# Optimization experiments

Hardware: AMD Instinct MI355X
Metric: run time of the kernel (lower is better)

## Reference

```python
import jax, jax.numpy as jnp
import numpy as np

B, S, K, D, H, COND, MR = 4, 1024, 1024, 1024, 16, 1024, 4
HD = D // H  # 64
INV_SQRT_HD = 1.0 / float(np.sqrt(HD))
GELU_C = 0.7978845608028654  # sqrt(2/pi)


def _make_rope(seqlen):
    pos = jnp.arange(seqlen, dtype=jnp.float32)
    inv = 1.0 / (10000.0 ** (jnp.arange(0, HD // 2, dtype=jnp.float32) * 2.0 / HD))
    ang = pos[:, None] * inv[None, :]                     # [S, HD/2]
    cos = jnp.concatenate([jnp.cos(ang), jnp.cos(ang)], -1)  # [S, HD]
    sin = jnp.concatenate([jnp.sin(ang), jnp.sin(ang)], -1)
    return cos[None, :, None, :], sin[None, :, None, :]   # [1,S,1,HD]


def setup_inputs():
    key = jax.random.key(0)
    ks = jax.random.split(key, 14)
    rn = lambda k, shape, s=0.02: jax.random.normal(k, shape, jnp.float32) * s
    cos_q, sin_q = _make_rope(S)
    cos_k, sin_k = _make_rope(K)
    ada_b = jnp.zeros((6 * D,), jnp.float32)
    ada_b = ada_b.at[2 * D:3 * D].set(0.5).at[5 * D:6 * D].set(0.5)  # gate_msa, gate_mlp init
    return {
        "q_x": jax.random.normal(ks[0], (B, S, D), jnp.float32),
        "kv_x": jax.random.normal(ks[1], (B, K, D), jnp.float32),
        "t_cond": jax.random.normal(ks[2], (B, COND), jnp.float32),
        "cos_q": cos_q, "sin_q": sin_q, "cos_k": cos_k, "sin_k": sin_k,
        "group_idxs": jax.random.randint(ks[3], (B, S), 0, 4, jnp.int32),
        "query_enabled": jax.random.randint(ks[4], (B, S), 0, 2, jnp.int32).astype(bool),
        "qn_w": jnp.ones((D,), jnp.float32),
        "kvn_w": jnp.ones((D,), jnp.float32),
        "n2_w": jnp.ones((D,), jnp.float32),
        "Wq": rn(ks[5], (D, D)), "Wkv": rn(ks[6], (D, 2 * D)), "Wo": rn(ks[7], (D, D)),
        "W1": rn(ks[8], (D, MR * D)), "b1": jnp.zeros((MR * D,), jnp.float32),
        "W2": rn(ks[9], (MR * D, D)), "b2": jnp.zeros((D,), jnp.float32),
        "adaW": rn(ks[10], (COND, 6 * D)), "adab": ada_b,
    }


def layer_norm(x, w):
    mu = jnp.mean(x, -1, keepdims=True)
    var = jnp.var(x, -1, keepdims=True)
    return (x - mu) * jax.lax.rsqrt(var + 1e-5) * w


def rope(x, cos, sin):
    # x: [B,S,H,HD]; cos/sin: [1,S,1,HD]; rotate_half convention
    x1, x2 = jnp.split(x, 2, axis=-1)
    return x * cos + jnp.concatenate([-x2, x1], -1) * sin


def gelu_tanh(x):
    return 0.5 * x * (1.0 + jnp.tanh(GELU_C * (x + 0.044715 * x * x * x)))


def reference(q_x, kv_x, t_cond, cos_q, sin_q, cos_k, sin_k, group_idxs, query_enabled,
              qn_w, kvn_w, n2_w, Wq, Wkv, Wo, W1, b1, W2, b2, adaW, adab):
    # adaLN modulation (inference: dropout disabled -> bias_dropout_add_scale = scale*x + residual)
    mod = (t_cond @ adaW + adab)[:, None, :]               # [B,1,6D]
    sh_msa, sc_msa, g_msa, sh_mlp, sc_mlp, g_mlp = jnp.split(mod, 6, axis=-1)

    qn = layer_norm(q_x, qn_w)
    kvn = layer_norm(kv_x, kvn_w)
    qn = qn * (1.0 + sc_msa) + sh_msa                      # modulate_fused

    q = (qn @ Wq).reshape(B, S, H, HD)
    kv = (kvn @ Wkv).reshape(B, K, 2, H, HD)
    k, v = kv[:, :, 0], kv[:, :, 1]
    q = rope(q, cos_q, sin_q)
    k = rope(k, cos_k, sin_k)

    # group cross-attn mask: attend only where groups differ
    attend = group_idxs[:, :, None] != group_idxs[:, None, :]  # [B,S,K]
    scores = jnp.einsum('bqhd,bkhd->bhqk', q, k) * INV_SQRT_HD
    scores = jnp.where(attend[:, None, :, :], scores, -1e9)
    p = jax.nn.softmax(scores, axis=-1)
    attn = jnp.einsum('bhqk,bkhd->bqhd', p, v).reshape(B, S, D)

    x = g_msa * (attn @ Wo) + q_x                          # fused bias-dropout-add-scale (inference)
    gate = query_enabled[..., None].astype(x.dtype)
    x = x * gate + q_x * (1.0 - gate)                      # gated_update

    x_mid = x
    h = layer_norm(x, n2_w) * (1.0 + sc_mlp) + sh_mlp
    h = gelu_tanh(h @ W1 + b1) @ W2 + b2
    x = g_mlp * h + x_mid
    x = x * gate + x_mid * (1.0 - gate)
    return x
```

## Files before the change

### kernel.cpp

```cpp
#include <hip/hip_runtime.h>
#include <hip/hip_bf16.h>
#include <math.h>

typedef __bf16 bf16_t;
typedef __attribute__((ext_vector_type(8))) __bf16 bf16x8;
typedef __attribute__((ext_vector_type(4))) float f32x4;

__global__ __launch_bounds__(256) void mod_init_kernel(
    const float* __restrict__ adab, float* __restrict__ mod)
{
  int i = blockIdx.x * 256 + threadIdx.x;
  int b = i / 6144, c = i - b * 6144;
  mod[i] = adab[c];
  (void)b;
}

__global__ __launch_bounds__(256) void mod_partial_kernel(
    const float* __restrict__ tc, const float* __restrict__ adaW,
    float* __restrict__ mod)
{
  __shared__ float st[4][128];
  int tid = threadIdx.x, z = blockIdx.y;
  for (int i = tid; i < 512; i += 256)
    st[i >> 7][i & 127] = tc[(i >> 7) * 1024 + z * 128 + (i & 127)];
  __syncthreads();
  int col = blockIdx.x * 256 + tid;
  float a0 = 0.f, a1 = 0.f, a2 = 0.f, a3 = 0.f;
  for (int k = 0; k < 128; ++k) {
    float wv = adaW[(size_t)(z * 128 + k) * 6144 + col];
    a0 = fmaf(st[0][k], wv, a0);
    a1 = fmaf(st[1][k], wv, a1);
    a2 = fmaf(st[2][k], wv, a2);
    a3 = fmaf(st[3][k], wv, a3);
  }
  atomicAdd(&mod[col], a0);
  atomicAdd(&mod[6144 + col], a1);
  atomicAdd(&mod[2 * 6144 + col], a2);
  atomicAdd(&mod[3 * 6144 + col], a3);
}

__global__ __launch_bounds__(256) void transpose_to_bf16(
    const float* __restrict__ in, bf16_t* __restrict__ out, int R, int C)
{
  __shared__ float tile[32][33];
  int c0 = blockIdx.x * 32, r0 = blockIdx.y * 32;
  int tx = threadIdx.x, ty = threadIdx.y;
#pragma unroll
  for (int i = 0; i < 4; ++i)
    tile[ty + i * 8][tx] = in[(size_t)(r0 + ty + i * 8) * C + c0 + tx];
  __syncthreads();
#pragma unroll
  for (int i = 0; i < 4; ++i)
    out[(size_t)(c0 + ty + i * 8) * R + r0 + tx] = (bf16_t)tile[tx][ty + i * 8];
}

__global__ __launch_bounds__(256) void ln_mod_kernel(
    const float* __restrict__ x, const float* __restrict__ wgt,
    const float* __restrict__ mod, int useMod, int shOff, int scOff,
    bf16_t* __restrict__ out)
{
  int row = blockIdx.x;
  int b = row >> 10;
  int tid = threadIdx.x;
  const float* xr = x + (size_t)row * 1024;
  float4 v = ((const float4*)xr)[tid];
  float s = v.x + v.y + v.z + v.w;
  float s2 = v.x * v.x + v.y * v.y + v.z * v.z + v.w * v.w;
#pragma unroll
  for (int off = 32; off > 0; off >>= 1) {
    s += __shfl_down(s, off, 64);
    s2 += __shfl_down(s2, off, 64);
  }
  __shared__ float ps[4], ps2[4];
  if ((tid & 63) == 0) { ps[tid >> 6] = s; ps2[tid >> 6] = s2; }
  __syncthreads();
  float mu = (ps[0] + ps[1] + ps[2] + ps[3]) * (1.0f / 1024.0f);
  float var = (ps2[0] + ps2[1] + ps2[2] + ps2[3]) * (1.0f / 1024.0f) - mu * mu;
  float rs = rsqrtf(var + 1e-5f);
  float xv[4] = {v.x, v.y, v.z, v.w};
#pragma unroll
  for (int i = 0; i < 4; ++i) {
    int col = tid * 4 + i;
    float n = (xv[i] - mu) * rs * wgt[col];
    if (useMod)
      n = n * (1.0f + mod[b * 6144 + scOff + col]) + mod[b * 6144 + shOff + col];
    out[(size_t)row * 1024 + col] = (bf16_t)n;
  }
}

__global__ __launch_bounds__(256) void reduce_q_rope_kernel(
    const float* __restrict__ P0, const float* __restrict__ P1,
    const float* __restrict__ cosq, const float* __restrict__ sinq,
    bf16_t* __restrict__ qr)
{
  int t = blockIdx.x * 256 + threadIdx.x;
  int hd = t & 31;
  int h = (t >> 5) & 15;
  int s = (t >> 9) & 1023;
  int b = t >> 19;
  size_t base = ((size_t)(b * 1024 + s)) * 1024 + h * 64 + hd;
  float v1 = P0[base] + P1[base];
  float v2 = P0[base + 32] + P1[base + 32];
  float c1 = cosq[s * 64 + hd], s1 = sinq[s * 64 + hd];
  float c2 = cosq[s * 64 + hd + 32], s2 = sinq[s * 64 + hd + 32];
  float o1 = (v1 * c1 - v2 * s1) * 0.125f;
  float o2 = (v2 * c2 + v1 * s2) * 0.125f;
  size_t ob = ((size_t)(b * 16 + h) * 1024 + s) * 64 + hd;
  qr[ob] = (bf16_t)o1;
  qr[ob + 32] = (bf16_t)o2;
}

__global__ __launch_bounds__(256) void reduce_kv_kernel(
    const float* __restrict__ P0, const float* __restrict__ P1,
    const float* __restrict__ cosk, const float* __restrict__ sink,
    bf16_t* __restrict__ kr, bf16_t* __restrict__ vt)
{
  __shared__ float ks[64][65];
  __shared__ float vs[64][65];
  int bh = blockIdx.x;
  int b = bh >> 4, h = bh & 15;
  int n0 = blockIdx.y * 64;
  int tid = threadIdx.x;
#pragma unroll
  for (int it = 0; it < 16; ++it) {
    int linear = tid + it * 256;
    int nl = linear >> 6, hd = linear & 63;
    size_t gi = ((size_t)(b * 1024 + n0 + nl)) * 2048 + h * 64 + hd;
    ks[nl][hd] = P0[gi] + P1[gi];
    vs[hd][nl] = P0[gi + 1024] + P1[gi + 1024];
  }
  __syncthreads();
#pragma unroll
  for (int it = 0; it < 16; ++it) {
    int linear = tid + it * 256;
    int nl = linear >> 6, hd = linear & 63;
    float kv = ks[nl][hd];
    float pv = ks[nl][hd ^ 32];
    float c = cosk[(n0 + nl) * 64 + hd], sn = sink[(n0 + nl) * 64 + hd];
    float o = (hd < 32) ? (kv * c - pv * sn) : (kv * c + pv * sn);
    kr[((size_t)bh * 1024 + n0 + nl) * 64 + hd] = (bf16_t)o;
    int rh = linear >> 6, nn = linear & 63;
    vt[((size_t)bh * 64 + rh) * 1024 + n0 + nn] = (bf16_t)vs[rh][nn];
  }
}

__global__ __launch_bounds__(256, 2) void attn_kernel(
    const bf16_t* __restrict__ qr, const bf16_t* __restrict__ kr,
    const bf16_t* __restrict__ vt, const int* __restrict__ grp,
    bf16_t* __restrict__ outp)
{
  __shared__ bf16_t Ks[64 * 72];
  __shared__ bf16_t Vs[64 * 72];
  __shared__ bf16_t Ps[128 * 72];
  __shared__ int gk[64];
  const int bh = blockIdx.x;
  const int b = bh >> 4, h = bh & 15;
  const int qBase = blockIdx.y * 128;
  const int tid = threadIdx.x, lane = tid & 63, w = tid >> 6;
  const int l15 = lane & 15, l4 = lane >> 4;
  const f32x4 zero = {0.f, 0.f, 0.f, 0.f};

  bf16x8 qA0[2], qA1[2];
  int gqr[2][4];
#pragma unroll
  for (int s = 0; s < 2; ++s) {
    int row = qBase + w * 32 + s * 16;
    const bf16_t* qp = qr + ((size_t)bh * 1024 + row + l15) * 64;
    qA0[s] = *(const bf16x8*)(qp + l4 * 8);
    qA1[s] = *(const bf16x8*)(qp + 32 + l4 * 8);
#pragma unroll
    for (int r = 0; r < 4; ++r) gqr[s][r] = grp[b * 1024 + row + l4 * 4 + r];
  }

  f32x4 oacc[2][4];
  float rsum[2][4];
#pragma unroll
  for (int s = 0; s < 2; ++s)
#pragma unroll
    for (int i = 0; i < 4; ++i) { oacc[s][i] = zero; rsum[s][i] = 0.f; }

  for (int kt = 0; kt < 16; ++kt) {
    __syncthreads();
#pragma unroll
    for (int i = 0; i < 2; ++i) {
      int c = tid * 2 + i;
      int r = c >> 3, cc = (c & 7) * 8;
      *(bf16x8*)(Ks + r * 72 + cc) =
          *(const bf16x8*)(kr + ((size_t)bh * 1024 + kt * 64 + r) * 64 + cc);
      *(bf16x8*)(Vs + r * 72 + cc) =
          *(const bf16x8*)(vt + ((size_t)bh * 64 + r) * 1024 + kt * 64 + cc);
    }
    if (tid < 64) gk[tid] = grp[b * 1024 + kt * 64 + tid];
    __syncthreads();

    int gkv[4];
    bf16x8 kf0[4], kf1[4];
#pragma unroll
    for (int nt = 0; nt < 4; ++nt) {
      gkv[nt] = gk[nt * 16 + l15];
      kf0[nt] = *(const bf16x8*)(Ks + (nt * 16 + l15) * 72 + l4 * 8);
      kf1[nt] = *(const bf16x8*)(Ks + (nt * 16 + l15) * 72 + 32 + l4 * 8);
    }

#pragma unroll
    for (int s = 0; s < 2; ++s) {
      f32x4 sacc[4];
#pragma unroll
      for (int nt = 0; nt < 4; ++nt) sacc[nt] = zero;
#pragma unroll
      for (int nt = 0; nt < 4; ++nt) {
        sacc[nt] = __builtin_amdgcn_mfma_f32_16x16x32_bf16(qA0[s], kf0[nt], sacc[nt], 0, 0, 0);
        sacc[nt] = __builtin_amdgcn_mfma_f32_16x16x32_bf16(qA1[s], kf1[nt], sacc[nt], 0, 0, 0);
      }
#pragma unroll
      for (int r = 0; r < 4; ++r) {
        int gq = gqr[s][r];
        float acc = 0.f;
#pragma unroll
        for (int nt = 0; nt < 4; ++nt) {
          float sv = sacc[nt][r] + ((gq == gkv[nt]) ? -60.f : 0.f);
          float p = __expf(sv);
          acc += p;
          Ps[(w * 32 + s * 16 + l4 * 4 + r) * 72 + nt * 16 + l15] = (bf16_t)p;
        }
        rsum[s][r] += acc;
      }
    }
    __syncthreads();
#pragma unroll
    for (int s = 0; s < 2; ++s) {
      const bf16_t* pp = Ps + (w * 32 + s * 16 + l15) * 72;
      bf16x8 pf0 = *(const bf16x8*)(pp + l4 * 8);
      bf16x8 pf1 = *(const bf16x8*)(pp + 32 + l4 * 8);
#pragma unroll
      for (int nt = 0; nt < 4; ++nt) {
        bf16x8 vf0 = *(const bf16x8*)(Vs + (nt * 16 + l15) * 72 + l4 * 8);
        bf16x8 vf1 = *(const bf16x8*)(Vs + (nt * 16 + l15) * 72 + 32 + l4 * 8);
        oacc[s][nt] = __builtin_amdgcn_mfma_f32_16x16x32_bf16(pf0, vf0, oacc[s][nt], 0, 0, 0);
        oacc[s][nt] = __builtin_amdgcn_mfma_f32_16x16x32_bf16(pf1, vf1, oacc[s][nt], 0, 0, 0);
      }
    }
  }

#pragma unroll
  for (int s = 0; s < 2; ++s)
#pragma unroll
    for (int r = 0; r < 4; ++r) {
      float t = rsum[s][r];
      t += __shfl_xor(t, 1, 64);
      t += __shfl_xor(t, 2, 64);
      t += __shfl_xor(t, 4, 64);
      t += __shfl_xor(t, 8, 64);
      rsum[s][r] = 1.f / t;
    }
#pragma unroll
  for (int s = 0; s < 2; ++s)
#pragma unroll
    for (int r = 0; r < 4; ++r) {
      int srow = qBase + w * 32 + s * 16 + l4 * 4 + r;
      float inv = rsum[s][r];
#pragma unroll
      for (int nt = 0; nt < 4; ++nt)
        outp[((size_t)(b * 1024 + srow)) * 1024 + h * 64 + nt * 16 + l15] =
            (bf16_t)(oacc[s][nt][r] * inv);
    }
}

__device__ __forceinline__ void stage16(const bf16_t* gp, bf16_t* lp) {
  __builtin_amdgcn_global_load_lds(
      (__attribute__((address_space(1))) void*)gp,
      (__attribute__((address_space(3))) void*)lp, 16, 0, 0);
}

template <int EPI>
__global__ __launch_bounds__(256, 2) void gemm_bt(
    const bf16_t* __restrict__ A, const bf16_t* __restrict__ Bt,
    int M, int N, int Kd, int kChunk,
    float* __restrict__ Cf, bf16_t* __restrict__ Cb,
    const float* __restrict__ bias)
{
  __shared__ bf16_t sA[128 * 32];
  __shared__ bf16_t sB[128 * 32];
  const int tid = threadIdx.x;
  const int lane = tid & 63, w = tid >> 6;
  const int wr = w >> 1, wc = w & 1;
  const int rowBase = blockIdx.y * 128;
  const int colBase = blockIdx.x * 128;
  const int l15 = lane & 15, l4 = lane >> 4;
  const int sr = lane >> 2;
  const int scc = (((lane & 3) ^ ((sr >> 1) & 3))) * 8;
  const int l4s = l4 ^ ((l15 >> 1) & 3);

  const f32x4 zero = {0.f, 0.f, 0.f, 0.f};
  f32x4 acc[4][4];
#pragma unroll
  for (int i = 0; i < 4; ++i)
#pragma unroll
    for (int j = 0; j < 4; ++j) acc[i][j] = zero;

  const bf16_t* aBase = A + (size_t)(rowBase + w * 32 + sr) * Kd + scc;
  const bf16_t* bBase = Bt + (size_t)(colBase + w * 32 + sr) * Kd + scc;

  const int kStart = blockIdx.z * kChunk;
  for (int k0 = kStart; k0 < kStart + kChunk; k0 += 32) {
    __syncthreads();
#pragma unroll
    for (int i = 0; i < 2; ++i) {
      stage16(aBase + (size_t)i * 16 * Kd + k0, sA + (w * 32 + i * 16) * 32);
      stage16(bBase + (size_t)i * 16 * Kd + k0, sB + (w * 32 + i * 16) * 32);
    }
    __syncthreads();
    bf16x8 af[4], bfr[4];
#pragma unroll
    for (int mt = 0; mt < 4; ++mt)
      af[mt] = *(const bf16x8*)(sA + (wr * 64 + mt * 16 + l15) * 32 + l4s * 8);
#pragma unroll
    for (int nt = 0; nt < 4; ++nt)
      bfr[nt] = *(const bf16x8*)(sB + (wc * 64 + nt * 16 + l15) * 32 + l4s * 8);
#pragma unroll
    for (int mt = 0; mt < 4; ++mt)
#pragma unroll
      for (int nt = 0; nt < 4; ++nt)
        acc[mt][nt] = __builtin_amdgcn_mfma_f32_16x16x32_bf16(af[mt], bfr[nt],
                                                              acc[mt][nt], 0, 0, 0);
  }

  const size_t zOff = (size_t)blockIdx.z * M * N;
#pragma unroll
  for (int mt = 0; mt < 4; ++mt) {
#pragma unroll
    for (int nt = 0; nt < 4; ++nt) {
      int col = colBase + wc * 64 + nt * 16 + l15;
#pragma unroll
      for (int r = 0; r < 4; ++r) {
        int rr = rowBase + wr * 64 + mt * 16 + l4 * 4 + r;
        float v = acc[mt][nt][r];
        if constexpr (EPI == 1) {
          float t = v + bias[col];
          float g = 0.5f * t *
                    (1.0f + tanhf(0.7978845608028654f * (t + 0.044715f * t * t * t)));
          Cb[(size_t)rr * N + col] = (bf16_t)g;
        } else {
          Cf[zOff + (size_t)rr * N + col] = v;
        }
      }
    }
  }
}

__global__ __launch_bounds__(256) void ln2_fused_kernel(
    const float* __restrict__ P0, const float* __restrict__ P1,
    const float* __restrict__ qx, const float* __restrict__ n2w,
    const float* __restrict__ mod, const int* __restrict__ qen,
    float* __restrict__ xbuf, bf16_t* __restrict__ xnmod)
{
  int row = blockIdx.x;
  int b = row >> 10;
  int tid = threadIdx.x;
  bool en = qen[row] != 0;
  float4 p0 = ((const float4*)(P0 + (size_t)row * 1024))[tid];
  float4 p1 = ((const float4*)(P1 + (size_t)row * 1024))[tid];
  float4 res = ((const float4*)(qx + (size_t)row * 1024))[tid];
  float4 g = ((const float4*)(mod + b * 6144 + 2048))[tid];
  float4 x;
  x.x = en ? fmaf(g.x, p0.x + p1.x, res.x) : res.x;
  x.y = en ? fmaf(g.y, p0.y + p1.y, res.y) : res.y;
  x.z = en ? fmaf(g.z, p0.z + p1.z, res.z) : res.z;
  x.w = en ? fmaf(g.w, p0.w + p1.w, res.w) : res.w;
  ((float4*)(xbuf + (size_t)row * 1024))[tid] = x;

  float s = x.x + x.y + x.z + x.w;
  float s2 = x.x * x.x + x.y * x.y + x.z * x.z + x.w * x.w;
#pragma unroll
  for (int off = 32; off > 0; off >>= 1) {
    s += __shfl_down(s, off, 64);
    s2 += __shfl_down(s2, off, 64);
  }
  __shared__ float ps[4], ps2[4];
  if ((tid & 63) == 0) { ps[tid >> 6] = s; ps2[tid >> 6] = s2; }
  __syncthreads();
  float mu = (ps[0] + ps[1] + ps[2] + ps[3]) * (1.0f / 1024.0f);
  float var = (ps2[0] + ps2[1] + ps2[2] + ps2[3]) * (1.0f / 1024.0f) - mu * mu;
  float rs = rsqrtf(var + 1e-5f);
  float4 sc = ((const float4*)(mod + b * 6144 + 4096))[tid];
  float4 sh = ((const float4*)(mod + b * 6144 + 3072))[tid];
  float4 wv = ((const float4*)n2w)[tid];
  float xv[4] = {x.x, x.y, x.z, x.w};
  float scv[4] = {sc.x, sc.y, sc.z, sc.w};
  float shv[4] = {sh.x, sh.y, sh.z, sh.w};
  float wvv[4] = {wv.x, wv.y, wv.z, wv.w};
#pragma unroll
  for (int i = 0; i < 4; ++i) {
    float n = (xv[i] - mu) * rs * wvv[i];
    n = n * (1.0f + scv[i]) + shv[i];
    xnmod[(size_t)row * 1024 + tid * 4 + i] = (bf16_t)n;
  }
}

__global__ __launch_bounds__(256) void final_reduce_kernel(
    const float* __restrict__ P, const float* __restrict__ b2,
    const float* __restrict__ mod, const int* __restrict__ qen,
    const float* __restrict__ xbuf, float* __restrict__ out)
{
  int row = blockIdx.x;
  int b = row >> 10;
  int tid = threadIdx.x;
  bool en = qen[row] != 0;
  size_t ro = (size_t)row * 1024;
  float4 p0 = ((const float4*)(P + ro))[tid];
  float4 p1 = ((const float4*)(P + 4194304 + ro))[tid];
  float4 p2 = ((const float4*)(P + 2 * 4194304 + ro))[tid];
  float4 p3 = ((const float4*)(P + 3 * 4194304 + ro))[tid];
  float4 bb = ((const float4*)b2)[tid];
  float4 xm = ((const float4*)(xbuf + ro))[tid];
  float4 g = ((const float4*)(mod + b * 6144 + 5120))[tid];
  float4 o;
  o.x = en ? fmaf(g.x, p0.x + p1.x + p2.x + p3.x + bb.x, xm.x) : xm.x;
  o.y = en ? fmaf(g.y, p0.y + p1.y + p2.y + p3.y + bb.y, xm.y) : xm.y;
  o.z = en ? fmaf(g.z, p0.z + p1.z + p2.z + p3.z + bb.z, xm.z) : xm.z;
  o.w = en ? fmaf(g.w, p0.w + p1.w + p2.w + p3.w + bb.w, xm.w) : xm.w;
  ((float4*)(out + ro))[tid] = o;
}

extern "C" void kernel_launch(void* const* d_in, const int* in_sizes, int n_in,
                              void* d_out, int out_size, void* d_ws, size_t ws_size,
                              hipStream_t stream)
{
  const float* q_x    = (const float*)d_in[0];
  const float* kv_x   = (const float*)d_in[1];
  const float* t_cond = (const float*)d_in[2];
  const float* cos_q  = (const float*)d_in[3];
  const float* sin_q  = (const float*)d_in[4];
  const float* cos_k  = (const float*)d_in[5];
  const float* sin_k  = (const float*)d_in[6];
  const int*   grp    = (const int*)d_in[7];
  const int*   qen    = (const int*)d_in[8];
  const float* qn_w   = (const float*)d_in[9];
  const float* kvn_w  = (const float*)d_in[10];
  const float* n2_w   = (const float*)d_in[11];
  const float* Wq     = (const float*)d_in[12];
  const float* Wkv    = (const float*)d_in[13];
  const float* Wo     = (const float*)d_in[14];
  const float* W1     = (const float*)d_in[15];
  const float* b1     = (const float*)d_in[16];
  const float* W2     = (const float*)d_in[17];
  const float* b2     = (const float*)d_in[18];
  const float* adaW   = (const float*)d_in[19];
  const float* adab   = (const float*)d_in[20];
  float* out = (float*)d_out;

  char* ws = (char*)d_ws;
  const size_t MB = 1ull << 20;
  float*  mod    = (float*)(ws + 0);
  bf16_t* Wq_t   = (bf16_t*)(ws + 98304);
  bf16_t* Wkv_t  = (bf16_t*)(ws + 98304 + 2 * MB);
  bf16_t* Wo_t   = (bf16_t*)(ws + 98304 + 6 * MB);
  bf16_t* W1_t   = (bf16_t*)(ws + 98304 + 8 * MB);
  bf16_t* W2_t   = (bf16_t*)(ws + 98304 + 16 * MB);
  bf16_t* qn_mod = (bf16_t*)(ws + 98304 + 24 * MB);
  bf16_t* kvn    = (bf16_t*)(ws + 98304 + 32 * MB);
  bf16_t* q_r    = (bf16_t*)(ws + 98304 + 40 * MB);
  bf16_t* k_r    = (bf16_t*)(ws + 98304 + 48 * MB);
  bf16_t* v_t    = (bf16_t*)(ws + 98304 + 56 * MB);
  bf16_t* h1     = (bf16_t*)(ws + 98304 + 64 * MB);
  float*  scr    = (float*)(ws + 98304 + 96 * MB);
  bf16_t* xn_mod = qn_mod;
  bf16_t* attn_o = kvn;
  float*  xbuf   = (float*)q_r;

  mod_init_kernel<<<96, 256, 0, stream>>>(adab, mod);
  mod_partial_kernel<<<dim3(24, 8), 256, 0, stream>>>(t_cond, adaW, mod);
  transpose_to_bf16<<<dim3(32, 32),  dim3(32, 8), 0, stream>>>(Wq,  Wq_t,  1024, 1024);
  transpose_to_bf16<<<dim3(64, 32),  dim3(32, 8), 0, stream>>>(Wkv, Wkv_t, 1024, 2048);
  transpose_to_bf16<<<dim3(32, 32),  dim3(32, 8), 0, stream>>>(Wo,  Wo_t,  1024, 1024);
  transpose_to_bf16<<<dim3(128, 32), dim3(32, 8), 0, stream>>>(W1,  W1_t,  1024, 4096);
  transpose_to_bf16<<<dim3(32, 128), dim3(32, 8), 0, stream>>>(W2,  W2_t,  4096, 1024);
  ln_mod_kernel<<<4096, 256, 0, stream>>>(q_x,  qn_w,  mod, 1, 0, 1024, qn_mod);
  ln_mod_kernel<<<4096, 256, 0, stream>>>(kv_x, kvn_w, mod, 0, 0, 0,    kvn);
  gemm_bt<4><<<dim3(8, 32, 2), 256, 0, stream>>>(qn_mod, Wq_t, 4096, 1024, 1024, 512,
                                                 scr, nullptr, nullptr);
  reduce_q_rope_kernel<<<8192, 256, 0, stream>>>(scr, scr + 4194304, cos_q, sin_q, q_r);
  gemm_bt<4><<<dim3(16, 32, 2), 256, 0, stream>>>(kvn, Wkv_t, 4096, 2048, 1024, 512,
                                                  scr, nullptr, nullptr);
  reduce_kv_kernel<<<dim3(64, 16), 256, 0, stream>>>(scr, scr + 8388608, cos_k, sin_k,
                                                     k_r, v_t);
  attn_kernel<<<dim3(64, 8), 256, 0, stream>>>(q_r, k_r, v_t, grp, attn_o);
  gemm_bt<4><<<dim3(8, 32, 2), 256, 0, stream>>>(attn_o, Wo_t, 4096, 1024, 1024, 512,
                                                 scr, nullptr, nullptr);
  ln2_fused_kernel<<<4096, 256, 0, stream>>>(scr, scr + 4194304, q_x, n2_w, mod, qen,
                                             xbuf, xn_mod);
  gemm_bt<1><<<dim3(32, 32, 1), 256, 0, stream>>>(xn_mod, W1_t, 4096, 4096, 1024, 1024,
                                                  nullptr, h1, b1);
  gemm_bt<4><<<dim3(8, 32, 4), 256, 0, stream>>>(h1, W2_t, 4096, 1024, 4096, 1024,
                                                 scr, nullptr, nullptr);
  final_reduce_kernel<<<4096, 256, 0, stream>>>(scr, b2, mod, qen, xbuf, out);
}
```

Before: 484.0 us.

## Store split-K partials in bf16, remap GEMM tiles per XCD, use exp-based GELU

Split-K GEMM partial outputs are now written and read as bf16 instead of fp32, halving scratch traffic for all reduce/epilogue kernels. The GEMM block index is remapped so blocks landing on the same XCD cover a contiguous region of tiles, aiming for better L2 reuse. The GELU tanh is replaced by an __expf-based formula. Storing partials in bf16 before summation loses precision, and the tile remapping assumes grid dimensions divisible by 8, 4 and 2.

```diff
diff --git a/kernel.cpp b/kernel.cpp
--- a/kernel.cpp
+++ b/kernel.cpp
@@ -4,6 +4,7 @@
 
 typedef __bf16 bf16_t;
 typedef __attribute__((ext_vector_type(8))) __bf16 bf16x8;
+typedef __attribute__((ext_vector_type(4))) __bf16 bf16x4;
 typedef __attribute__((ext_vector_type(4))) float f32x4;
 
 __global__ __launch_bounds__(256) void mod_init_kernel(
@@ -89,7 +90,7 @@
 }
 
 __global__ __launch_bounds__(256) void reduce_q_rope_kernel(
-    const float* __restrict__ P0, const float* __restrict__ P1,
+    const bf16_t* __restrict__ P0, const bf16_t* __restrict__ P1,
     const float* __restrict__ cosq, const float* __restrict__ sinq,
     bf16_t* __restrict__ qr)
 {
@@ -99,8 +100,8 @@
   int s = (t >> 9) & 1023;
   int b = t >> 19;
   size_t base = ((size_t)(b * 1024 + s)) * 1024 + h * 64 + hd;
-  float v1 = P0[base] + P1[base];
-  float v2 = P0[base + 32] + P1[base + 32];
+  float v1 = (float)P0[base] + (float)P1[base];
+  float v2 = (float)P0[base + 32] + (float)P1[base + 32];
   float c1 = cosq[s * 64 + hd], s1 = sinq[s * 64 + hd];
   float c2 = cosq[s * 64 + hd + 32], s2 = sinq[s * 64 + hd + 32];
   float o1 = (v1 * c1 - v2 * s1) * 0.125f;
@@ -111,7 +112,7 @@
 }
 
 __global__ __launch_bounds__(256) void reduce_kv_kernel(
-    const float* __restrict__ P0, const float* __restrict__ P1,
+    const bf16_t* __restrict__ P0, const bf16_t* __restrict__ P1,
     const float* __restrict__ cosk, const float* __restrict__ sink,
     bf16_t* __restrict__ kr, bf16_t* __restrict__ vt)
 {
@@ -126,8 +127,8 @@
     int linear = tid + it * 256;
     int nl = linear >> 6, hd = linear & 63;
     size_t gi = ((size_t)(b * 1024 + n0 + nl)) * 2048 + h * 64 + hd;
-    ks[nl][hd] = P0[gi] + P1[gi];
-    vs[hd][nl] = P0[gi + 1024] + P1[gi + 1024];
+    ks[nl][hd] = (float)P0[gi] + (float)P1[gi];
+    vs[hd][nl] = (float)P0[gi + 1024] + (float)P1[gi + 1024];
   }
   __syncthreads();
 #pragma unroll
@@ -276,7 +277,7 @@
 __global__ __launch_bounds__(256, 2) void gemm_bt(
     const bf16_t* __restrict__ A, const bf16_t* __restrict__ Bt,
     int M, int N, int Kd, int kChunk,
-    float* __restrict__ Cf, bf16_t* __restrict__ Cb,
+    bf16_t* __restrict__ Cb,
     const float* __restrict__ bias)
 {
   __shared__ bf16_t sA[128 * 32];
@@ -284,8 +285,16 @@
   const int tid = threadIdx.x;
   const int lane = tid & 63, w = tid >> 6;
   const int wr = w >> 1, wc = w & 1;
-  const int rowBase = blockIdx.y * 128;
-  const int colBase = blockIdx.x * 128;
+
+  const int gx = gridDim.x, gy = gridDim.y;
+  const int L = blockIdx.y * gx + blockIdx.x;
+  const int xcd = L & 7, idx = L >> 3;
+  const int ry = gy >> 2, rx = gx >> 1;
+  const int tileY = (xcd & 3) * ry + (idx % ry);
+  const int tileX = (xcd >> 2) * rx + (idx / ry);
+  const int rowBase = tileY * 128;
+  const int colBase = tileX * 128;
+
   const int l15 = lane & 15, l4 = lane >> 4;
   const int sr = lane >> 2;
   const int scc = (((lane & 3) ^ ((sr >> 1) & 3))) * 8;
@@ -337,11 +346,12 @@
         float v = acc[mt][nt][r];
         if constexpr (EPI == 1) {
           float t = v + bias[col];
-          float g = 0.5f * t *
-                    (1.0f + tanhf(0.7978845608028654f * (t + 0.044715f * t * t * t)));
+          float z = 0.7978845608028654f * (t + 0.044715f * t * t * t);
+          float e = __expf(2.f * z);
+          float g = 0.5f * t * (2.f - 2.f / (e + 1.f));
           Cb[(size_t)rr * N + col] = (bf16_t)g;
         } else {
-          Cf[zOff + (size_t)rr * N + col] = v;
+          Cb[zOff + (size_t)rr * N + col] = (bf16_t)v;
         }
       }
     }
@@ -349,7 +359,7 @@
 }
 
 __global__ __launch_bounds__(256) void ln2_fused_kernel(
-    const float* __restrict__ P0, const float* __restrict__ P1,
+    const bf16_t* __restrict__ P0, const bf16_t* __restrict__ P1,
     const float* __restrict__ qx, const float* __restrict__ n2w,
     const float* __restrict__ mod, const int* __restrict__ qen,
     float* __restrict__ xbuf, bf16_t* __restrict__ xnmod)
@@ -358,15 +368,15 @@
   int b = row >> 10;
   int tid = threadIdx.x;
   bool en = qen[row] != 0;
-  float4 p0 = ((const float4*)(P0 + (size_t)row * 1024))[tid];
-  float4 p1 = ((const float4*)(P1 + (size_t)row * 1024))[tid];
+  bf16x4 p0 = *(const bf16x4*)(P0 + (size_t)row * 1024 + tid * 4);
+  bf16x4 p1 = *(const bf16x4*)(P1 + (size_t)row * 1024 + tid * 4);
   float4 res = ((const float4*)(qx + (size_t)row * 1024))[tid];
   float4 g = ((const float4*)(mod + b * 6144 + 2048))[tid];
   float4 x;
-  x.x = en ? fmaf(g.x, p0.x + p1.x, res.x) : res.x;
-  x.y = en ? fmaf(g.y, p0.y + p1.y, res.y) : res.y;
-  x.z = en ? fmaf(g.z, p0.z + p1.z, res.z) : res.z;
-  x.w = en ? fmaf(g.w, p0.w + p1.w, res.w) : res.w;
+  x.x = en ? fmaf(g.x, (float)p0[0] + (float)p1[0], res.x) : res.x;
+  x.y = en ? fmaf(g.y, (float)p0[1] + (float)p1[1], res.y) : res.y;
+  x.z = en ? fmaf(g.z, (float)p0[2] + (float)p1[2], res.z) : res.z;
+  x.w = en ? fmaf(g.w, (float)p0[3] + (float)p1[3], res.w) : res.w;
   ((float4*)(xbuf + (size_t)row * 1024))[tid] = x;
 
   float s = x.x + x.y + x.z + x.w;
@@ -398,7 +408,7 @@
 }
 
 __global__ __launch_bounds__(256) void final_reduce_kernel(
-    const float* __restrict__ P, const float* __restrict__ b2,
+    const bf16_t* __restrict__ P, const float* __restrict__ b2,
     const float* __restrict__ mod, const int* __restrict__ qen,
     const float* __restrict__ xbuf, float* __restrict__ out)
 {
@@ -406,20 +416,24 @@
   int b = row >> 10;
   int tid = threadIdx.x;
   bool en = qen[row] != 0;
-  size_t ro = (size_t)row * 1024;
-  float4 p0 = ((const float4*)(P + ro))[tid];
-  float4 p1 = ((const float4*)(P + 4194304 + ro))[tid];
-  float4 p2 = ((const float4*)(P + 2 * 4194304 + ro))[tid];
-  float4 p3 = ((const float4*)(P + 3 * 4194304 + ro))[tid];
+  size_t ro = (size_t)row * 1024 + tid * 4;
+  bf16x4 p0 = *(const bf16x4*)(P + ro);
+  bf16x4 p1 = *(const bf16x4*)(P + 4194304 + ro);
+  bf16x4 p2 = *(const bf16x4*)(P + 2 * 4194304 + ro);
+  bf16x4 p3 = *(const bf16x4*)(P + 3 * 4194304 + ro);
   float4 bb = ((const float4*)b2)[tid];
-  float4 xm = ((const float4*)(xbuf + ro))[tid];
+  float4 xm = *(const float4*)(xbuf + ro);
   float4 g = ((const float4*)(mod + b * 6144 + 5120))[tid];
   float4 o;
-  o.x = en ? fmaf(g.x, p0.x + p1.x + p2.x + p3.x + bb.x, xm.x) : xm.x;
-  o.y = en ? fmaf(g.y, p0.y + p1.y + p2.y + p3.y + bb.y, xm.y) : xm.y;
-  o.z = en ? fmaf(g.z, p0.z + p1.z + p2.z + p3.z + bb.z, xm.z) : xm.z;
-  o.w = en ? fmaf(g.w, p0.w + p1.w + p2.w + p3.w + bb.w, xm.w) : xm.w;
-  ((float4*)(out + ro))[tid] = o;
+  float v0 = (float)p0[0] + (float)p1[0] + (float)p2[0] + (float)p3[0] + bb.x;
+  float v1 = (float)p0[1] + (float)p1[1] + (float)p2[1] + (float)p3[1] + bb.y;
+  float v2 = (float)p0[2] + (float)p1[2] + (float)p2[2] + (float)p3[2] + bb.z;
+  float v3 = (float)p0[3] + (float)p1[3] + (float)p2[3] + (float)p3[3] + bb.w;
+  o.x = en ? fmaf(g.x, v0, xm.x) : xm.x;
+  o.y = en ? fmaf(g.y, v1, xm.y) : xm.y;
+  o.z = en ? fmaf(g.z, v2, xm.z) : xm.z;
+  o.w = en ? fmaf(g.w, v3, xm.w) : xm.w;
+  *(float4*)(out + ro) = o;
 }
 
 extern "C" void kernel_launch(void* const* d_in, const int* in_sizes, int n_in,
@@ -463,7 +477,7 @@
   bf16_t* k_r    = (bf16_t*)(ws + 98304 + 48 * MB);
   bf16_t* v_t    = (bf16_t*)(ws + 98304 + 56 * MB);
   bf16_t* h1     = (bf16_t*)(ws + 98304 + 64 * MB);
-  float*  scr    = (float*)(ws + 98304 + 96 * MB);
+  bf16_t* scr    = (bf16_t*)(ws + 98304 + 96 * MB);
   bf16_t* xn_mod = qn_mod;
   bf16_t* attn_o = kvn;
   float*  xbuf   = (float*)q_r;
@@ -478,20 +492,20 @@
   ln_mod_kernel<<<4096, 256, 0, stream>>>(q_x,  qn_w,  mod, 1, 0, 1024, qn_mod);
   ln_mod_kernel<<<4096, 256, 0, stream>>>(kv_x, kvn_w, mod, 0, 0, 0,    kvn);
   gemm_bt<4><<<dim3(8, 32, 2), 256, 0, stream>>>(qn_mod, Wq_t, 4096, 1024, 1024, 512,
-                                                 scr, nullptr, nullptr);
+                                                 scr, nullptr);
   reduce_q_rope_kernel<<<8192, 256, 0, stream>>>(scr, scr + 4194304, cos_q, sin_q, q_r);
   gemm_bt<4><<<dim3(16, 32, 2), 256, 0, stream>>>(kvn, Wkv_t, 4096, 2048, 1024, 512,
-                                                  scr, nullptr, nullptr);
+                                                  scr, nullptr);
   reduce_kv_kernel<<<dim3(64, 16), 256, 0, stream>>>(scr, scr + 8388608, cos_k, sin_k,
                                                      k_r, v_t);
   attn_kernel<<<dim3(64, 8), 256, 0, stream>>>(q_r, k_r, v_t, grp, attn_o);
   gemm_bt<4><<<dim3(8, 32, 2), 256, 0, stream>>>(attn_o, Wo_t, 4096, 1024, 1024, 512,
-                                                 scr, nullptr, nullptr);
+                                                 scr, nullptr);
   ln2_fused_kernel<<<4096, 256, 0, stream>>>(scr, scr + 4194304, q_x, n2_w, mod, qen,
                                              xbuf, xn_mod);
   gemm_bt<1><<<dim3(32, 32, 1), 256, 0, stream>>>(xn_mod, W1_t, 4096, 4096, 1024, 1024,
-                                                  nullptr, h1, b1);
+                                                  h1, b1);
   gemm_bt<4><<<dim3(8, 32, 4), 256, 0, stream>>>(h1, W2_t, 4096, 1024, 4096, 1024,
-                                                 scr, nullptr, nullptr);
+                                                 scr, nullptr);
   final_reduce_kernel<<<4096, 256, 0, stream>>>(scr, b2, mod, qen, xbuf, out);
 }
```

After: 451.2 us. 1.07x faster.
